# Kernel tuning notes

Measured on AMD Instinct MI355X. Metric: run time of the kernel, lower is better.

The kernel has to match this reference:

```python
import jax, jax.numpy as jnp
import numpy as np

B, L, D, V, T = 4, 512, 2048, 32000, 1024


def setup_inputs() -> dict:
    key = jax.random.key(0)
    k1, k2, k3 = jax.random.split(key, 3)
    encoder_outs = jax.random.normal(k1, (B, L, D), dtype=jnp.float32)
    embed_weight = jax.random.normal(k2, (V, D), dtype=jnp.float32) * 0.02
    input_ids = jax.random.randint(k3, (B, T), 0, V)
    # encoder (audio) tokens occupy the prefix of the LLM input sequence
    modality_mask = jnp.broadcast_to(jnp.arange(T) < L, (B, T))
    return {
        "encoder_outs": encoder_outs,
        "embed_weight": embed_weight,
        "input_ids": input_ids,
        "modality_mask": modality_mask,
    }


def reference(encoder_outs, embed_weight, input_ids, modality_mask):
    # chunked matmul in torch == one big contraction: (B,L,D) x (V,D) -> (B,L,V)
    sim = jnp.einsum("bld,vd->blv", encoder_outs, embed_weight)
    enc_norm = jnp.sqrt(jnp.sum(jnp.square(encoder_outs), axis=-1, keepdims=True))
    w_norm = jnp.sqrt(jnp.sum(jnp.square(embed_weight), axis=-1))  # (V,)
    cosine = sim / enc_norm / w_norm[None, None, :]
    quantize_index = jnp.argmax(cosine, axis=-1)  # (B, L)
    enc_quant = embed_weight[quantize_index]      # (B, L, D) gather lookup

    inputs_embeds = embed_weight[input_ids]       # (B, T, D)
    # pad encoder tokens to full sequence length, then blend via modality mask
    enc_pad = jnp.pad(enc_quant, ((0, 0), (0, T - L), (0, 0)))
    blended = jnp.where(modality_mask[:, :, None], enc_pad, inputs_embeds)
    return blended, quantize_index
```

## Files before the change

kernel.cpp:

```cpp
#include <hip/hip_runtime.h>
#include <math.h>

typedef __attribute__((ext_vector_type(8))) short short8v;
typedef __attribute__((ext_vector_type(4))) float f32x4;
typedef unsigned long long u64;
typedef unsigned short ushort_t;

constexpr int Bb = 4;
constexpr int Ll = 512;
constexpr int Dk = 2048;
constexpr int Vv = 32000;
constexpr int Tt = 1024;
constexpr int Mrows = Bb * Ll;

constexpr int BM = 256;
constexpr int BN = 256;
constexpr int BK = 32;
constexpr int NKT = Dk / BK;
constexpr int NBX = Mrows / BM;
constexpr int NBY = Vv / BN;
constexpr int NWG = NBX * NBY;
constexpr int CHUNK = NWG / 8;

constexpr int KCAND = 8;
constexpr int CAND_STRIDE = 500;

constexpr int FBM = 128;
constexpr int FBN = 128;
constexpr int FNVB = Vv / FBN;

constexpr size_t WS_NEEDED = 147914752ull;

__device__ __forceinline__ unsigned int fkey(float f) {
    unsigned int u = __float_as_uint(f);
    return (u & 0x80000000u) ? ~u : (u | 0x80000000u);
}
__device__ __forceinline__ void top2(u64& b1, u64& b2, u64 p) {
    if (p > b1) { b2 = b1; b1 = p; }
    else if (p > b2) { b2 = p; }
}
__device__ __forceinline__ u64 shfl64(u64 x, int m) {
    unsigned lo = __shfl_xor((unsigned)x, m, 64);
    unsigned hi = __shfl_xor((unsigned)(x >> 32), m, 64);
    return ((u64)hi << 32) | lo;
}
__device__ __forceinline__ ushort_t bftrunc(float x) {
    return (ushort_t)(__float_as_uint(x) >> 16);
}
__device__ __forceinline__ void gload_lds16(const void* g, void* l) {
    __builtin_amdgcn_global_load_lds(
        (const __attribute__((address_space(1))) unsigned int*)g,
        (__attribute__((address_space(3))) unsigned int*)l, 16, 0, 0);
}

__global__ __launch_bounds__(256) void convertA_kernel(const float* __restrict__ A,
                                                       ushort_t* __restrict__ Ab) {
    int i = blockIdx.x * blockDim.x + threadIdx.x;
    const float4* src = (const float4*)A;
    float4 x = src[i * 2], y = src[i * 2 + 1];
    ushort_t o[8] = {bftrunc(x.x), bftrunc(x.y), bftrunc(x.z), bftrunc(x.w),
                     bftrunc(y.x), bftrunc(y.y), bftrunc(y.z), bftrunc(y.w)};
    *(int4*)(Ab + (size_t)i * 8) = *(const int4*)o;
}

__global__ __launch_bounds__(256) void convertW_kernel(const float* __restrict__ W,
                                                       ushort_t* __restrict__ Wb,
                                                       float* __restrict__ winv) {
    int wave = (blockIdx.x * blockDim.x + threadIdx.x) >> 6;
    int lane = threadIdx.x & 63;
    if (wave >= Vv) return;
    const float4* row = (const float4*)(W + (size_t)wave * Dk);
    ushort4* orow = (ushort4*)(Wb + (size_t)wave * Dk);
    float s = 0.f;
#pragma unroll
    for (int i = 0; i < Dk / 4 / 64; ++i) {
        float4 v = row[lane + 64 * i];
        s = fmaf(v.x, v.x, s); s = fmaf(v.y, v.y, s);
        s = fmaf(v.z, v.z, s); s = fmaf(v.w, v.w, s);
        ushort4 o;
        o.x = bftrunc(v.x); o.y = bftrunc(v.y);
        o.z = bftrunc(v.z); o.w = bftrunc(v.w);
        orow[lane + 64 * i] = o;
    }
#pragma unroll
    for (int off = 32; off; off >>= 1) s += __shfl_down(s, off, 64);
    if (lane == 0) winv[wave] = 1.0f / sqrtf(s);
}

__global__ __launch_bounds__(256) void wnorm_kernel(const float* __restrict__ W,
                                                    float* __restrict__ winv) {
    int wave = (blockIdx.x * blockDim.x + threadIdx.x) >> 6;
    int lane = threadIdx.x & 63;
    if (wave >= Vv) return;
    const float4* row = (const float4*)(W + (size_t)wave * Dk);
    float s = 0.f;
#pragma unroll
    for (int i = 0; i < Dk / 4 / 64; ++i) {
        float4 v = row[lane + 64 * i];
        s = fmaf(v.x, v.x, s); s = fmaf(v.y, v.y, s);
        s = fmaf(v.z, v.z, s); s = fmaf(v.w, v.w, s);
    }
#pragma unroll
    for (int off = 32; off; off >>= 1) s += __shfl_down(s, off, 64);
    if (lane == 0) winv[wave] = 1.0f / sqrtf(s);
}

__global__ void init_best_kernel(u64* __restrict__ best) {
    int i = blockIdx.x * blockDim.x + threadIdx.x;
    if (i < Mrows) best[i] = 0ull;
}

__global__ __launch_bounds__(1024, 4) void score_topk_kernel(
    const ushort_t* __restrict__ Ab, const ushort_t* __restrict__ Wb,
    const float* __restrict__ winv, u64* __restrict__ cand) {
    __shared__ __align__(16) ushort_t Alds[2][8192];
    __shared__ __align__(16) ushort_t Wlds[2][8192];

    const int orig = blockIdx.x;
    const int swz = (orig & 7) * CHUNK + (orig >> 3);
    const int bx = swz & (NBX - 1);
    const int by = swz >> 3;
    const int row0 = bx * BM;
    const int v0 = by * BN;

    const int tid = threadIdx.x;
    const int lane = tid & 63;
    const int w = tid >> 6;
    const int wrr = w >> 2;
    const int wcc = w & 3;

    const int rsub = lane & 15;
    const int ksub = (lane >> 4) * 8;

    const ushort_t* sA = Ab + (size_t)(row0 + w * 16 + rsub) * Dk + ksub;
    const ushort_t* sW = Wb + (size_t)(v0 + w * 16 + rsub) * Dk + ksub;

    f32x4 acc[4][4];
#pragma unroll
    for (int i = 0; i < 4; ++i)
#pragma unroll
        for (int j = 0; j < 4; ++j) acc[i][j] = (f32x4){0.f, 0.f, 0.f, 0.f};

    gload_lds16(sA, &Alds[0][w * 512]);
    gload_lds16(sW, &Wlds[0][w * 512]);
    __syncthreads();

    int cur = 0;
    for (int t = 0; t < NKT; ++t) {
        if (t + 1 < NKT) {
            const int k0 = (t + 1) * BK;
            gload_lds16(sA + k0, &Alds[cur ^ 1][w * 512]);
            gload_lds16(sW + k0, &Wlds[cur ^ 1][w * 512]);
        }
        const short8v* Ap = (const short8v*)&Alds[cur][0];
        const short8v* Wp = (const short8v*)&Wlds[cur][0];
        short8v a[4], b[4];
#pragma unroll
        for (int m = 0; m < 4; ++m) a[m] = Ap[(wrr * 4 + m) * 64 + lane];
#pragma unroll
        for (int n = 0; n < 4; ++n) b[n] = Wp[(wcc * 4 + n) * 64 + lane];
        __builtin_amdgcn_s_setprio(1);
#pragma unroll
        for (int m = 0; m < 4; ++m)
#pragma unroll
            for (int n = 0; n < 4; ++n)
                acc[m][n] = __builtin_amdgcn_mfma_f32_16x16x32_bf16(a[m], b[n],
                                                                    acc[m][n], 0, 0, 0);
        __builtin_amdgcn_s_setprio(0);
        __syncthreads();
        cur ^= 1;
    }

    const int cb = lane & 15;
    float wv[4];
#pragma unroll
    for (int n = 0; n < 4; ++n) wv[n] = winv[v0 + wcc * 64 + n * 16 + cb];

    u64(*red)[8] = (u64(*)[8]) & Alds[0][0];
#pragma unroll
    for (int m = 0; m < 4; ++m) {
#pragma unroll
        for (int reg = 0; reg < 4; ++reg) {
            u64 b1 = 0, b2 = 0;
#pragma unroll
            for (int n = 0; n < 4; ++n) {
                float s = acc[m][n][reg] * wv[n];
                int v = v0 + wcc * 64 + n * 16 + cb;
                u64 p = ((u64)fkey(s) << 32) | (unsigned)(Vv - 1 - v);
                top2(b1, b2, p);
            }
#pragma unroll
            for (int msk = 1; msk < 16; msk <<= 1) {
                u64 o1 = shfl64(b1, msk);
                u64 o2 = shfl64(b2, msk);
                top2(b1, b2, o1);
                top2(b1, b2, o2);
            }
            if (cb == 0) {
                int rl = wrr * 64 + m * 16 + ((lane >> 4) << 2) + reg;
                red[rl][wcc * 2] = b1;
                red[rl][wcc * 2 + 1] = b2;
            }
        }
    }
    __syncthreads();
    if (tid < BM) {
        u64 b1 = red[tid][0], b2 = red[tid][1];
#pragma unroll
        for (int j = 2; j < 8; ++j) top2(b1, b2, red[tid][j]);
        u64* c = cand + (size_t)(row0 + tid) * CAND_STRIDE + by * 2;
        c[0] = b1;
        c[1] = b2;
    }
}

template <typename LdsT>
__device__ __forceinline__ void topk_epilogue_f(f32x4 (&acc)[4][4], LdsT* ldsbase,
                                                const float* __restrict__ winv,
                                                u64* __restrict__ cand, int row0, int v0,
                                                int vby, int tid, int lane, int wr,
                                                int wc) {
    const int cbase = v0 + wc * 64 + (lane & 15);
    float wv[4];
#pragma unroll
    for (int nf = 0; nf < 4; ++nf) wv[nf] = winv[cbase + nf * 16];

    u64(*red)[4] = (u64(*)[4])ldsbase;
#pragma unroll
    for (int mf = 0; mf < 4; ++mf) {
#pragma unroll
        for (int reg = 0; reg < 4; ++reg) {
            u64 b1 = 0, b2 = 0;
#pragma unroll
            for (int nf = 0; nf < 4; ++nf) {
                float s = acc[mf][nf][reg] * wv[nf];
                int v = cbase + nf * 16;
                u64 p = ((u64)fkey(s) << 32) | (unsigned)(Vv - 1 - v);
                top2(b1, b2, p);
            }
#pragma unroll
            for (int m = 1; m < 16; m <<= 1) {
                u64 o1 = shfl64(b1, m);
                u64 o2 = shfl64(b2, m);
                top2(b1, b2, o1);
                top2(b1, b2, o2);
            }
            if ((lane & 15) == 0) {
                int rl = wr * 64 + mf * 16 + ((lane >> 4) << 2) + reg;
                red[rl][wc * 2] = b1;
                red[rl][wc * 2 + 1] = b2;
            }
        }
    }
    __syncthreads();
    if (tid < FBM) {
        u64 b1 = red[tid][0], b2 = red[tid][1];
        top2(b1, b2, red[tid][2]);
        top2(b1, b2, red[tid][3]);
        u64* c = cand + (size_t)(row0 + tid) * CAND_STRIDE + vby * 2;
        c[0] = b1;
        c[1] = b2;
    }
}

__global__ __launch_bounds__(256) void score_topk_fallback(
    const float* __restrict__ A, const float* __restrict__ W,
    const float* __restrict__ winv, u64* __restrict__ cand) {
    __shared__ __align__(16) short Albuf[4096];
    __shared__ __align__(16) short Wlbuf[4096];

    const int tid = threadIdx.x;
    const int row0 = blockIdx.x * FBM;
    const int v0 = blockIdx.y * FBN;
    const int lane = tid & 63;
    const int wid = tid >> 6;
    const int wr = wid >> 1, wc = wid & 1;

    const int rA = ((tid >> 6) << 4) + (tid & 15);
    const int kk = ((tid >> 4) & 3) * 8;

    const float* pa = A + (size_t)(row0 + rA) * Dk + kk;
    const float* pw = W + (size_t)(v0 + rA) * Dk + kk;

    float4 fa0, fa1, fa2, fa3, fw0, fw1, fw2, fw3;
    auto ld4 = [](const float* p) { return *(const float4*)p; };
    auto load_regs = [&](int k0) {
        fa0 = ld4(pa + k0); fa1 = ld4(pa + k0 + 4);
        fa2 = ld4(pa + k0 + (size_t)64 * Dk); fa3 = ld4(pa + k0 + (size_t)64 * Dk + 4);
        fw0 = ld4(pw + k0); fw1 = ld4(pw + k0 + 4);
        fw2 = ld4(pw + k0 + (size_t)64 * Dk); fw3 = ld4(pw + k0 + (size_t)64 * Dk + 4);
    };
    auto pk = [](float lo, float hi) {
        return (int)((__float_as_uint(lo) >> 16) | (__float_as_uint(hi) & 0xFFFF0000u));
    };
    auto cv = [&](float4 a, float4 b) {
        int4 r; r.x = pk(a.x, a.y); r.y = pk(a.z, a.w);
        r.z = pk(b.x, b.y); r.w = pk(b.z, b.w); return r;
    };
    auto write_lds = [&]() {
        *(int4*)(Albuf + tid * 8) = cv(fa0, fa1);
        *(int4*)(Albuf + tid * 8 + 2048) = cv(fa2, fa3);
        *(int4*)(Wlbuf + tid * 8) = cv(fw0, fw1);
        *(int4*)(Wlbuf + tid * 8 + 2048) = cv(fw2, fw3);
    };

    f32x4 acc[4][4];
#pragma unroll
    for (int i = 0; i < 4; ++i)
#pragma unroll
        for (int j = 0; j < 4; ++j) acc[i][j] = (f32x4){0.f, 0.f, 0.f, 0.f};

    load_regs(0);
    for (int kt = 0; kt < Dk / 32; ++kt) {
        write_lds();
        __syncthreads();
        if (kt + 1 < Dk / 32) load_regs((kt + 1) * 32);
        short8v af[4], bf[4];
        const short8v* Ap = (const short8v*)Albuf;
        const short8v* Wp = (const short8v*)Wlbuf;
#pragma unroll
        for (int mf = 0; mf < 4; ++mf) af[mf] = Ap[(wr * 4 + mf) * 64 + lane];
#pragma unroll
        for (int nf = 0; nf < 4; ++nf) bf[nf] = Wp[(wc * 4 + nf) * 64 + lane];
#pragma unroll
        for (int mf = 0; mf < 4; ++mf)
#pragma unroll
            for (int nf = 0; nf < 4; ++nf)
                acc[mf][nf] = __builtin_amdgcn_mfma_f32_16x16x32_bf16(
                    af[mf], bf[nf], acc[mf][nf], 0, 0, 0);
        __syncthreads();
    }

    topk_epilogue_f(acc, Albuf, winv, cand, row0, v0, blockIdx.y, tid, lane, wr, wc);
}

__global__ __launch_bounds__(256) void topk_kernel(const u64* __restrict__ cand,
                                                   int* __restrict__ sel, int nents) {
    int row = blockIdx.x * 4 + (threadIdx.x >> 6);
    int lane = threadIdx.x & 63;
    if (row >= Mrows) return;
    const u64* c = cand + (size_t)row * CAND_STRIDE;
    u64 v[8];
#pragma unroll
    for (int i = 0; i < 8; ++i) {
        int idx = lane + i * 64;
        v[i] = (idx < nents) ? c[idx] : 0ull;
    }
#pragma unroll
    for (int it = 0; it < KCAND; ++it) {
        u64 lm = 0;
#pragma unroll
        for (int i = 0; i < 8; ++i) lm = v[i] > lm ? v[i] : lm;
#pragma unroll
        for (int m = 32; m; m >>= 1) {
            u64 o = shfl64(lm, m);
            lm = o > lm ? o : lm;
        }
#pragma unroll
        for (int i = 0; i < 8; ++i)
            if (v[i] == lm) v[i] = 0;
        if (lane == 0) sel[row * KCAND + it] = Vv - 1 - (int)(unsigned)(lm & 0xFFFFFFFFu);
    }
}

__global__ __launch_bounds__(256) void rescore_kernel(
    const float* __restrict__ A, const float* __restrict__ W,
    const float* __restrict__ winv, const int* __restrict__ sel,
    u64* __restrict__ best) {
    int gw = (int)((blockIdx.x * blockDim.x + threadIdx.x) >> 6);
    int lane = threadIdx.x & 63;
    if (gw >= Mrows * KCAND) return;
    int row = gw >> 3, c = gw & 7;
    int v = sel[row * KCAND + c];
    const float4* a = (const float4*)(A + (size_t)row * Dk);
    const float4* w = (const float4*)(W + (size_t)v * Dk);
    float s = 0.f;
#pragma unroll
    for (int i = 0; i < Dk / 4 / 64; ++i) {
        float4 x = a[lane + 64 * i], y = w[lane + 64 * i];
        s = fmaf(x.x, y.x, s); s = fmaf(x.y, y.y, s);
        s = fmaf(x.z, y.z, s); s = fmaf(x.w, y.w, s);
    }
#pragma unroll
    for (int m = 32; m; m >>= 1) s += __shfl_xor(s, m, 64);
    if (lane == 0) {
        u64 p = ((u64)fkey(s * winv[v]) << 32) | (unsigned)(Vv - 1 - v);
        atomicMax(best + row, p);
    }
}

__global__ __launch_bounds__(256) void blend_kernel(
    const float* __restrict__ emb, const int* __restrict__ ids,
    const u64* __restrict__ best, float* __restrict__ out) {
    int row = blockIdx.x;
    int b = row / Tt;
    int t = row % Tt;
    int idx;
    if (t < Ll) {
        idx = Vv - 1 - (int)(best[b * Ll + t] & 0xFFFFFFFFu);
    } else {
        idx = ids[row];
    }
    const float4* src = (const float4*)(emb + (size_t)idx * Dk);
    float4* dst = (float4*)(out + (size_t)row * Dk);
    for (int i = threadIdx.x; i < Dk / 4; i += blockDim.x) dst[i] = src[i];
    if (t < Ll && threadIdx.x == 0) {
        out[(size_t)Bb * Tt * Dk + (size_t)(b * Ll + t)] = (float)idx;
    }
}

extern "C" void kernel_launch(void* const* d_in, const int* in_sizes, int n_in,
                              void* d_out, int out_size, void* d_ws, size_t ws_size,
                              hipStream_t stream) {
    const float* encoder_outs = (const float*)d_in[0];
    const float* embed_weight = (const float*)d_in[1];
    const int* input_ids = (const int*)d_in[2];

    float* out = (float*)d_out;

    float* winv = (float*)d_ws;
    u64* best = (u64*)((char*)d_ws + 131072);
    int* sel = (int*)((char*)d_ws + 147456);
    u64* cand = (u64*)((char*)d_ws + 262144);
    ushort_t* Abf = (ushort_t*)((char*)d_ws + 8454144);
    ushort_t* Wbf = (ushort_t*)((char*)d_ws + 16842752);

    init_best_kernel<<<(Mrows + 255) / 256, 256, 0, stream>>>(best);

    if (ws_size >= WS_NEEDED) {
        convertA_kernel<<<Mrows * Dk / 8 / 256, 256, 0, stream>>>(encoder_outs, Abf);
        convertW_kernel<<<Vv * 64 / 256, 256, 0, stream>>>(embed_weight, Wbf, winv);
        score_topk_kernel<<<NWG, 1024, 0, stream>>>(Abf, Wbf, winv, cand);
        topk_kernel<<<Mrows / 4, 256, 0, stream>>>(cand, sel, 2 * NBY);
    } else {
        wnorm_kernel<<<Vv * 64 / 256, 256, 0, stream>>>(embed_weight, winv);
        dim3 grid(Mrows / FBM, Vv / FBN);
        score_topk_fallback<<<grid, 256, 0, stream>>>(encoder_outs, embed_weight, winv,
                                                      cand);
        topk_kernel<<<Mrows / 4, 256, 0, stream>>>(cand, sel, 2 * FNVB);
    }
    rescore_kernel<<<Mrows * KCAND / 4, 256, 0, stream>>>(encoder_outs, embed_weight,
                                                          winv, sel, best);
    blend_kernel<<<Bb * Tt, 256, 0, stream>>>(embed_weight, input_ids, best, out);
}
```

Baseline: 1.074 ms.

## Switch candidate scoring GEMM to FP8 with pre-tiled MFMA-ready layouts

Replaces the bf16 conversion and GEMM in the candidate-scoring pass with FP8 e4m3 operands. The weights are scaled by 64 before quantization. The conversion kernels now write A and W pre-swizzled into contiguous per-K-tile blocks, so each tile load is one linear 16-byte copy into LDS, and BK grows to 64. This halves operand bytes and uses the faster fp8 MFMA. The cost is coarser approximate scores, which depend on the exact rescore stage recovering correct argmax candidates.

```diff
diff --git a/kernel.cpp b/kernel.cpp
--- a/kernel.cpp
+++ b/kernel.cpp
@@ -1,10 +1,12 @@
 #include <hip/hip_runtime.h>
+#include <hip/hip_fp8.h>
 #include <math.h>
 
 typedef __attribute__((ext_vector_type(8))) short short8v;
 typedef __attribute__((ext_vector_type(4))) float f32x4;
 typedef unsigned long long u64;
 typedef unsigned short ushort_t;
+typedef unsigned char u8;
 
 constexpr int Bb = 4;
 constexpr int Ll = 512;
@@ -15,12 +17,13 @@
 
 constexpr int BM = 256;
 constexpr int BN = 256;
-constexpr int BK = 32;
+constexpr int BK = 64;
 constexpr int NKT = Dk / BK;
 constexpr int NBX = Mrows / BM;
 constexpr int NBY = Vv / BN;
 constexpr int NWG = NBX * NBY;
 constexpr int CHUNK = NWG / 8;
+constexpr int TILE_BYTES = 32 * 512;
 
 constexpr int KCAND = 8;
 constexpr int CAND_STRIDE = 500;
@@ -29,7 +32,7 @@
 constexpr int FBN = 128;
 constexpr int FNVB = Vv / FBN;
 
-constexpr size_t WS_NEEDED = 147914752ull;
+constexpr size_t WS_NEEDED = 16842752ull + 65536000ull;
 
 __device__ __forceinline__ unsigned int fkey(float f) {
     unsigned int u = __float_as_uint(f);
@@ -44,8 +47,9 @@
     unsigned hi = __shfl_xor((unsigned)(x >> 32), m, 64);
     return ((u64)hi << 32) | lo;
 }
-__device__ __forceinline__ ushort_t bftrunc(float x) {
-    return (ushort_t)(__float_as_uint(x) >> 16);
+__device__ __forceinline__ u8 to_e4m3(float x) {
+    __hip_fp8_e4m3 q(x);
+    return q.__x;
 }
 __device__ __forceinline__ void gload_lds16(const void* g, void* l) {
     __builtin_amdgcn_global_load_lds(
@@ -53,38 +57,52 @@
         (__attribute__((address_space(3))) unsigned int*)l, 16, 0, 0);
 }
 
-__global__ __launch_bounds__(256) void convertA_kernel(const float* __restrict__ A,
-                                                       ushort_t* __restrict__ Ab) {
-    int i = blockIdx.x * blockDim.x + threadIdx.x;
-    const float4* src = (const float4*)A;
-    float4 x = src[i * 2], y = src[i * 2 + 1];
-    ushort_t o[8] = {bftrunc(x.x), bftrunc(x.y), bftrunc(x.z), bftrunc(x.w),
-                     bftrunc(y.x), bftrunc(y.y), bftrunc(y.z), bftrunc(y.w)};
-    *(int4*)(Ab + (size_t)i * 8) = *(const int4*)o;
-}
-
-__global__ __launch_bounds__(256) void convertW_kernel(const float* __restrict__ W,
-                                                       ushort_t* __restrict__ Wb,
-                                                       float* __restrict__ winv) {
-    int wave = (blockIdx.x * blockDim.x + threadIdx.x) >> 6;
-    int lane = threadIdx.x & 63;
-    if (wave >= Vv) return;
-    const float4* row = (const float4*)(W + (size_t)wave * Dk);
-    ushort4* orow = (ushort4*)(Wb + (size_t)wave * Dk);
-    float s = 0.f;
-#pragma unroll
-    for (int i = 0; i < Dk / 4 / 64; ++i) {
-        float4 v = row[lane + 64 * i];
-        s = fmaf(v.x, v.x, s); s = fmaf(v.y, v.y, s);
-        s = fmaf(v.z, v.z, s); s = fmaf(v.w, v.w, s);
-        ushort4 o;
-        o.x = bftrunc(v.x); o.y = bftrunc(v.y);
-        o.z = bftrunc(v.z); o.w = bftrunc(v.w);
-        orow[lane + 64 * i] = o;
-    }
-#pragma unroll
-    for (int off = 32; off; off >>= 1) s += __shfl_down(s, off, 64);
-    if (lane == 0) winv[wave] = 1.0f / sqrtf(s);
+__global__ __launch_bounds__(256) void convertA_fp8(const float* __restrict__ A,
+                                                    u8* __restrict__ At) {
+    const int row = blockIdx.x * 4 + (threadIdx.x >> 6);
+    const int lane = threadIdx.x & 63;
+    const int bx = row >> 8, rg = (row & 255) >> 4, r15 = row & 15;
+    const float* src = A + (size_t)row * Dk;
+#pragma unroll
+    for (int i = 0; i < 4; ++i) {
+        const int k0 = (i * 64 + lane) * 8;
+        float4 x = *(const float4*)(src + k0);
+        float4 y = *(const float4*)(src + k0 + 4);
+        u8 o[8] = {to_e4m3(x.x), to_e4m3(x.y), to_e4m3(x.z), to_e4m3(x.w),
+                   to_e4m3(y.x), to_e4m3(y.y), to_e4m3(y.z), to_e4m3(y.w)};
+        const int t = k0 >> 6, c = (k0 >> 5) & 1, lp = r15 + ((k0 >> 3) & 3) * 16;
+        *(u64*)(At + ((size_t)(bx * NKT + t) * 32 + rg * 2 + c) * 512 + lp * 8) =
+            *(const u64*)o;
+    }
+}
+
+__global__ __launch_bounds__(256) void convertW_fp8(const float* __restrict__ W,
+                                                    u8* __restrict__ Wt,
+                                                    float* __restrict__ winv) {
+    const int row = blockIdx.x * 4 + (threadIdx.x >> 6);
+    const int lane = threadIdx.x & 63;
+    const int by = row >> 8, rg = (row & 255) >> 4, r15 = row & 15;
+    const float* src = W + (size_t)row * Dk;
+    float sq = 0.f;
+#pragma unroll
+    for (int i = 0; i < 4; ++i) {
+        const int k0 = (i * 64 + lane) * 8;
+        float4 x = *(const float4*)(src + k0);
+        float4 y = *(const float4*)(src + k0 + 4);
+        sq = fmaf(x.x, x.x, sq); sq = fmaf(x.y, x.y, sq);
+        sq = fmaf(x.z, x.z, sq); sq = fmaf(x.w, x.w, sq);
+        sq = fmaf(y.x, y.x, sq); sq = fmaf(y.y, y.y, sq);
+        sq = fmaf(y.z, y.z, sq); sq = fmaf(y.w, y.w, sq);
+        u8 o[8] = {to_e4m3(x.x * 64.f), to_e4m3(x.y * 64.f), to_e4m3(x.z * 64.f),
+                   to_e4m3(x.w * 64.f), to_e4m3(y.x * 64.f), to_e4m3(y.y * 64.f),
+                   to_e4m3(y.z * 64.f), to_e4m3(y.w * 64.f)};
+        const int t = k0 >> 6, c = (k0 >> 5) & 1, lp = r15 + ((k0 >> 3) & 3) * 16;
+        *(u64*)(Wt + ((size_t)(by * NKT + t) * 32 + rg * 2 + c) * 512 + lp * 8) =
+            *(const u64*)o;
+    }
+#pragma unroll
+    for (int off = 32; off; off >>= 1) sq += __shfl_down(sq, off, 64);
+    if (lane == 0) winv[row] = 1.0f / sqrtf(sq);
 }
 
 __global__ __launch_bounds__(256) void wnorm_kernel(const float* __restrict__ W,
@@ -111,10 +129,10 @@
 }
 
 __global__ __launch_bounds__(1024, 4) void score_topk_kernel(
-    const ushort_t* __restrict__ Ab, const ushort_t* __restrict__ Wb,
+    const u8* __restrict__ At, const u8* __restrict__ Wt,
     const float* __restrict__ winv, u64* __restrict__ cand) {
-    __shared__ __align__(16) ushort_t Alds[2][8192];
-    __shared__ __align__(16) ushort_t Wlds[2][8192];
+    __shared__ __align__(16) u8 Alds[2][TILE_BYTES];
+    __shared__ __align__(16) u8 Wlds[2][TILE_BYTES];
 
     const int orig = blockIdx.x;
     const int swz = (orig & 7) * CHUNK + (orig >> 3);
@@ -129,11 +147,8 @@
     const int wrr = w >> 2;
     const int wcc = w & 3;
 
-    const int rsub = lane & 15;
-    const int ksub = (lane >> 4) * 8;
-
-    const ushort_t* sA = Ab + (size_t)(row0 + w * 16 + rsub) * Dk + ksub;
-    const ushort_t* sW = Wb + (size_t)(v0 + w * 16 + rsub) * Dk + ksub;
+    const u8* sA = At + (size_t)bx * NKT * TILE_BYTES + w * 1024 + lane * 16;
+    const u8* sW = Wt + (size_t)by * NKT * TILE_BYTES + w * 1024 + lane * 16;
 
     f32x4 acc[4][4];
 #pragma unroll
@@ -141,31 +156,34 @@
 #pragma unroll
         for (int j = 0; j < 4; ++j) acc[i][j] = (f32x4){0.f, 0.f, 0.f, 0.f};
 
-    gload_lds16(sA, &Alds[0][w * 512]);
-    gload_lds16(sW, &Wlds[0][w * 512]);
+    gload_lds16(sA, &Alds[0][w * 1024]);
+    gload_lds16(sW, &Wlds[0][w * 1024]);
     __syncthreads();
 
     int cur = 0;
     for (int t = 0; t < NKT; ++t) {
         if (t + 1 < NKT) {
-            const int k0 = (t + 1) * BK;
-            gload_lds16(sA + k0, &Alds[cur ^ 1][w * 512]);
-            gload_lds16(sW + k0, &Wlds[cur ^ 1][w * 512]);
+            const size_t off = (size_t)(t + 1) * TILE_BYTES;
+            gload_lds16(sA + off, &Alds[cur ^ 1][w * 1024]);
+            gload_lds16(sW + off, &Wlds[cur ^ 1][w * 1024]);
         }
-        const short8v* Ap = (const short8v*)&Alds[cur][0];
-        const short8v* Wp = (const short8v*)&Wlds[cur][0];
-        short8v a[4], b[4];
-#pragma unroll
-        for (int m = 0; m < 4; ++m) a[m] = Ap[(wrr * 4 + m) * 64 + lane];
-#pragma unroll
-        for (int n = 0; n < 4; ++n) b[n] = Wp[(wcc * 4 + n) * 64 + lane];
         __builtin_amdgcn_s_setprio(1);
 #pragma unroll
-        for (int m = 0; m < 4; ++m)
+        for (int c = 0; c < 2; ++c) {
+            long long a[4], b[4];
+#pragma unroll
+            for (int m = 0; m < 4; ++m)
+                a[m] = *(const long long*)&Alds[cur][(((wrr * 4 + m) * 2 + c) * 64 + lane) * 8];
 #pragma unroll
             for (int n = 0; n < 4; ++n)
-                acc[m][n] = __builtin_amdgcn_mfma_f32_16x16x32_bf16(a[m], b[n],
-                                                                    acc[m][n], 0, 0, 0);
+                b[n] = *(const long long*)&Wlds[cur][(((wcc * 4 + n) * 2 + c) * 64 + lane) * 8];
+#pragma unroll
+            for (int m = 0; m < 4; ++m)
+#pragma unroll
+                for (int n = 0; n < 4; ++n)
+                    acc[m][n] = __builtin_amdgcn_mfma_f32_16x16x32_fp8_fp8(
+                        a[m], b[n], acc[m][n], 0, 0, 0);
+        }
         __builtin_amdgcn_s_setprio(0);
         __syncthreads();
         cur ^= 1;
@@ -422,15 +440,15 @@
     u64* best = (u64*)((char*)d_ws + 131072);
     int* sel = (int*)((char*)d_ws + 147456);
     u64* cand = (u64*)((char*)d_ws + 262144);
-    ushort_t* Abf = (ushort_t*)((char*)d_ws + 8454144);
-    ushort_t* Wbf = (ushort_t*)((char*)d_ws + 16842752);
+    u8* At = (u8*)((char*)d_ws + 8454144);
+    u8* Wt = (u8*)((char*)d_ws + 16842752);
 
     init_best_kernel<<<(Mrows + 255) / 256, 256, 0, stream>>>(best);
 
     if (ws_size >= WS_NEEDED) {
-        convertA_kernel<<<Mrows * Dk / 8 / 256, 256, 0, stream>>>(encoder_outs, Abf);
-        convertW_kernel<<<Vv * 64 / 256, 256, 0, stream>>>(embed_weight, Wbf, winv);
-        score_topk_kernel<<<NWG, 1024, 0, stream>>>(Abf, Wbf, winv, cand);
+        convertA_fp8<<<Mrows / 4, 256, 0, stream>>>(encoder_outs, At);
+        convertW_fp8<<<Vv / 4, 256, 0, stream>>>(embed_weight, Wt, winv);
+        score_topk_kernel<<<NWG, 1024, 0, stream>>>(At, Wt, winv, cand);
         topk_kernel<<<Mrows / 4, 256, 0, stream>>>(cand, sel, 2 * NBY);
     } else {
         wnorm_kernel<<<Vv * 64 / 256, 256, 0, stream>>>(embed_weight, winv);
```

Result: faster. 947.6 us (-11.8%).
